# Optimization experiments

Measured on AMD Instinct MI355X. Metric: run time of the kernel, lower is better.

Reference implementation:

```python
import jax, jax.numpy as jnp
import numpy as np

EPS = 1e-6


def sparsemax(z):
    # sparsemax over last axis (Martins & Astudillo 2016)
    n = z.shape[-1]
    zs = -jnp.sort(-z, axis=-1)                      # sorted descending
    cum = jnp.cumsum(zs, axis=-1)
    k = jnp.arange(1, n + 1, dtype=z.dtype)
    support = (1.0 + k * zs) > cum                   # [..., n]
    ksup = jnp.sum(support, axis=-1, keepdims=True)  # support size (int)
    tau = (jnp.take_along_axis(cum, ksup - 1, axis=-1) - 1.0) / ksup.astype(z.dtype)
    return jnp.maximum(z - tau, 0.0)


def setup_inputs() -> dict:
    key = jax.random.key(0)
    k1, k2, k3, k4, k5, k6 = jax.random.split(key, 6)
    bi, bt, K, L, d = 128, 128, 36, 50, 1024
    img_cls = jax.random.normal(k1, (bi, d), dtype=jnp.float32)
    imgs = jax.random.normal(k2, (bi, K, d), dtype=jnp.float32)
    cap_cls = jax.random.normal(k3, (bt, d), dtype=jnp.float32)
    caps = jax.random.normal(k4, (bt, L, d), dtype=jnp.float32)
    img_lens = jax.random.randint(k5, (bi,), 18, K + 1).at[0].set(K)
    cap_lens = jax.random.randint(k6, (bt,), 25, L + 1).at[0].set(L)
    return {"img_cls": img_cls, "imgs": imgs, "cap_cls": cap_cls,
            "caps": caps, "img_lens": img_lens, "cap_lens": cap_lens}


def reference(img_cls, imgs, cap_cls, caps, img_lens, cap_lens):
    # forward_s2d: masked fine-grained sims -> sparsemax over flattened (K*L) -> weighted sum
    bi, K, d = imgs.shape
    bt, L, _ = caps.shape
    imgs = imgs + EPS
    caps = caps + EPS
    imgs = imgs / jnp.linalg.norm(imgs, axis=-1, keepdims=True)
    caps = caps / jnp.linalg.norm(caps, axis=-1, keepdims=True)
    fg = jnp.einsum('ikd,tld->itkl', imgs, caps)             # [bi,bt,K,L]
    rmask = jnp.arange(K)[None, :] < img_lens[:, None]        # [bi,K]
    cmask = jnp.arange(L)[None, :] < cap_lens[:, None]        # [bt,L]
    mask = rmask[:, None, :, None] & cmask[None, :, None, :]  # [bi,bt,K,L]
    fg = jnp.where(mask, fg, 0.0).reshape(bi, bt, K * L)
    attn = sparsemax(fg)
    return jnp.sum(fg * attn, axis=-1)                        # [bi,bt]
```

## Files before the change

kernel.cpp:

```cpp
#include <hip/hip_runtime.h>
#include <stdint.h>

#define EPSF 1e-6f

typedef unsigned short u16;
typedef __attribute__((ext_vector_type(8))) u16 u16x8;
typedef __attribute__((ext_vector_type(8))) __bf16 bf16x8;
typedef __attribute__((ext_vector_type(4))) float f32x4;

static constexpr int NBI = 128, NBT = 128, KI = 36, LC = 50, DD = 1024;
static constexpr int NEL = KI * LC;
static constexpr int GM  = NBI * KI;
static constexpr int GN  = NBT * LC;
static constexpr int BM = 256, BN = 256, BK = 64;
static constexpr int KT  = DD / BK;
static constexpr int MT  = GM / BM;
static constexpr int NTT = GN / BN;
static constexpr int TB  = BM * BK;

static __device__ __forceinline__ u16 f2bf(float f) {
  uint32_t u = __float_as_uint(f);
  u += 0x7fffu + ((u >> 16) & 1u);
  return (u16)(u >> 16);
}
static __device__ __forceinline__ float bf2f(u16 h) {
  return __uint_as_float((uint32_t)h << 16);
}

typedef __attribute__((address_space(1))) void gv_t;
typedef __attribute__((address_space(3))) void lv_t;
static __device__ __forceinline__ void gload16(const void* g, void* l) {
  __builtin_amdgcn_global_load_lds((const gv_t*)g, (lv_t*)l, 16, 0, 0);
}

__global__ __launch_bounds__(256) void hcam_normcast(
    const float* __restrict__ imgs, const float* __restrict__ caps,
    u16* __restrict__ A, u16* __restrict__ B) {
  int r = blockIdx.x;
  const float* src; u16* dst;
  if (r < GM) { src = imgs + (size_t)r * DD;        dst = A + (size_t)r * DD; }
  else        { src = caps + (size_t)(r - GM) * DD; dst = B + (size_t)(r - GM) * DD; }
  int tid = threadIdx.x;
  float4 v = *(const float4*)(src + tid * 4);
  v.x += EPSF; v.y += EPSF; v.z += EPSF; v.w += EPSF;
  float ss = v.x * v.x + v.y * v.y + v.z * v.z + v.w * v.w;
  #pragma unroll
  for (int m = 32; m; m >>= 1) ss += __shfl_xor(ss, m);
  __shared__ float wsum[4];
  if ((tid & 63) == 0) wsum[tid >> 6] = ss;
  __syncthreads();
  float inv = 1.0f / sqrtf(wsum[0] + wsum[1] + wsum[2] + wsum[3]);
  ushort4 o = make_ushort4(f2bf(v.x * inv), f2bf(v.y * inv), f2bf(v.z * inv), f2bf(v.w * inv));
  *(ushort4*)(dst + tid * 4) = o;
}

__global__ __launch_bounds__(512, 2) void hcam_gemm8(
    const u16* __restrict__ A, const u16* __restrict__ B, float* __restrict__ C) {
  __shared__ u16 As[2 * TB];
  __shared__ u16 Bs[2 * TB];

  const int nwg = MT * NTT;
  int orig = blockIdx.x;
  int qq = nwg >> 3, rr = nwg & 7;
  int xcd = orig & 7, idx = orig >> 3;
  int wg = (xcd < rr ? xcd * (qq + 1) : rr * (qq + 1) + (xcd - rr) * qq) + idx;
  const int bm = wg % MT, bn = wg / MT;

  const int tid = threadIdx.x, lane = tid & 63, w = tid >> 6;
  const int wm = w >> 2, wn = w & 3;
  const u16* Ag = A + (size_t)(bm * BM) * DD;
  const u16* Bg = B + (size_t)(bn * BN) * DD;

  const int srow = tid >> 3;
  const int sc16 = (tid & 7) ^ (srow & 7);
  const int wbase = w * 8;

  auto stage = [&](const u16* g, u16* lds, int kt, int h) {
    #pragma unroll
    for (int j = 0; j < 2; ++j) {
      int row = h * 128 + j * 64 + srow;
      gload16(g + (size_t)row * DD + kt * BK + sc16 * 8,
              lds + (h * 128 + j * 64 + wbase) * BK);
    }
  };

  f32x4 acc[8][4];
  #pragma unroll
  for (int i = 0; i < 8; ++i)
    #pragma unroll
    for (int j = 0; j < 4; ++j) acc[i][j] = (f32x4){0.f, 0.f, 0.f, 0.f};

  const int fr = lane & 15, g4 = lane >> 4;

  auto tile = [&](int t, u16* as_c, u16* bs_c, u16* as_n, u16* bs_n) {
    const int tn = t + 1;
    if (tn < KT) {
      stage(Ag, as_n, tn, 0);
      asm volatile("s_waitcnt vmcnt(2)" ::: "memory");
    } else {
      asm volatile("s_waitcnt vmcnt(0)" ::: "memory");
    }
    __builtin_amdgcn_s_barrier();
    __builtin_amdgcn_sched_barrier(0);
    #pragma unroll
    for (int ph = 0; ph < 4; ++ph) {
      const int mh = (ph == 0 || ph == 3) ? 0 : 1;
      const int nh = (ph >= 2) ? 1 : 0;
      bf16x8 af[2][4], bfv[2][2];
      #pragma unroll
      for (int k2 = 0; k2 < 2; ++k2) {
        const int c16 = k2 * 4 + g4;
        const int cs = (c16 ^ (fr & 7)) << 3;
        #pragma unroll
        for (int mi = 0; mi < 4; ++mi) {
          int rowl = wm * 128 + mh * 64 + mi * 16 + fr;
          af[k2][mi] = __builtin_bit_cast(bf16x8, *(const u16x8*)(as_c + rowl * BK + cs));
        }
        #pragma unroll
        for (int ni = 0; ni < 2; ++ni) {
          int rowl = wn * 64 + nh * 32 + ni * 16 + fr;
          bfv[k2][ni] = __builtin_bit_cast(bf16x8, *(const u16x8*)(bs_c + rowl * BK + cs));
        }
      }
      if (tn < KT) {
        if (ph == 0)      stage(Bg, bs_n, tn, 0);
        else if (ph == 1) stage(Ag, as_n, tn, 1);
        else if (ph == 2) stage(Bg, bs_n, tn, 1);
      }
      __builtin_amdgcn_s_setprio(1);
      #pragma unroll
      for (int k2 = 0; k2 < 2; ++k2)
        #pragma unroll
        for (int mi = 0; mi < 4; ++mi)
          #pragma unroll
          for (int ni = 0; ni < 2; ++ni)
            acc[mh * 4 + mi][nh * 2 + ni] = __builtin_amdgcn_mfma_f32_16x16x32_bf16(
                af[k2][mi], bfv[k2][ni], acc[mh * 4 + mi][nh * 2 + ni], 0, 0, 0);
      __builtin_amdgcn_s_setprio(0);
    }
    __builtin_amdgcn_s_barrier();
    __builtin_amdgcn_sched_barrier(0);
  };

  stage(Ag, As, 0, 0); stage(Ag, As, 0, 1);
  stage(Bg, Bs, 0, 0); stage(Bg, Bs, 0, 1);

  #pragma unroll 1
  for (int tp = 0; tp < KT; tp += 2) {
    tile(tp,     As,      Bs,      As + TB, Bs + TB);
    tile(tp + 1, As + TB, Bs + TB, As,      Bs);
  }

  const int fc = lane & 15, fq = (lane >> 4) * 4;
  #pragma unroll
  for (int am = 0; am < 8; ++am) {
    #pragma unroll
    for (int an = 0; an < 4; ++an) {
      const int row0 = bm * BM + wm * 128 + am * 16 + fq;
      const int col  = bn * BN + wn * 64 + an * 16 + fc;
      #pragma unroll
      for (int j = 0; j < 4; ++j)
        C[(size_t)(row0 + j) * GN + col] = acc[am][an][j];
    }
  }
}

static constexpr int RPT = (NEL + 63) / 64;

__global__ __launch_bounds__(256) void hcam_spmax_w(
    const float* __restrict__ C, const int* __restrict__ ilen, const int* __restrict__ clen,
    float* __restrict__ out) {
  const int wid  = blockIdx.x * 4 + (threadIdx.x >> 6);
  const int lane = threadIdx.x & 63;
  const int i = wid >> 7, t = wid & 127;
  const int il = ilen[i], cl = clen[t];
  const float* base = C + (size_t)i * KI * GN + t * LC;

  float v[RPT];
  float sum = 0.f;
  #pragma unroll
  for (int r = 0; r < RPT; ++r) {
    int p = lane + (r << 6);
    float x = -1e30f;
    if (p < NEL) {
      int k = p / LC, l = p - k * LC;
      if (k < il && l < cl) { x = base[(size_t)k * GN + l]; sum += x; }
    }
    v[r] = x;
  }
  #pragma unroll
  for (int m = 32; m; m >>= 1) sum += __shfl_xor(sum, m);

  const float mzero = (float)(NEL - il * cl);
  float tau  = (sum - 1.0f) * (1.0f / NEL);
  float prev = (float)NEL;
  for (int it = 0; it < 32; ++it) {
    float ss = 0.f, cc = 0.f;
    #pragma unroll
    for (int r = 0; r < RPT; ++r) {
      if (v[r] > tau) { ss += v[r]; cc += 1.0f; }
    }
    #pragma unroll
    for (int m = 32; m; m >>= 1) { ss += __shfl_xor(ss, m); cc += __shfl_xor(cc, m); }
    if (tau < 0.f) cc += mzero;
    if (cc == prev || cc < 1.0f) break;
    float tn = (ss - 1.0f) / cc;
    prev = cc;
    if (tn <= tau) break;
    tau = tn;
  }

  float o = 0.f;
  #pragma unroll
  for (int r = 0; r < RPT; ++r) {
    float d = v[r] - tau;
    if (d > 0.f) o += v[r] * d;
  }
  #pragma unroll
  for (int m = 32; m; m >>= 1) o += __shfl_xor(o, m);
  if (lane == 0) out[wid] = o;
}

static __device__ __forceinline__ void bred2(float& a, float& b2, int tid, float* red) {
  #pragma unroll
  for (int m = 32; m; m >>= 1) { a += __shfl_xor(a, m); b2 += __shfl_xor(b2, m); }
  __syncthreads();
  if ((tid & 63) == 0) { red[(tid >> 6) * 2] = a; red[(tid >> 6) * 2 + 1] = b2; }
  __syncthreads();
  a  = red[0] + red[2] + red[4] + red[6];
  b2 = red[1] + red[3] + red[5] + red[7];
}

static __device__ __forceinline__ void sparsemax_out(float vals[8], int tid, float* red, float* outp) {
  float s = 0.f, d = 0.f;
  #pragma unroll
  for (int r = 0; r < 8; ++r) { int p = tid + (r << 8); if (p < NEL) s += vals[r]; }
  bred2(s, d, tid, red);
  float tau  = (s - 1.0f) * (1.0f / NEL);
  float prev = (float)NEL;
  for (int it = 0; it < 64; ++it) {
    float ss = 0.f, cc = 0.f;
    #pragma unroll
    for (int r = 0; r < 8; ++r) {
      int p = tid + (r << 8);
      if (p < NEL && vals[r] > tau) { ss += vals[r]; cc += 1.0f; }
    }
    bred2(ss, cc, tid, red);
    if (cc == prev || cc < 1.0f) break;
    float tn = (ss - 1.0f) / cc;
    prev = cc;
    if (tn <= tau) break;
    tau = tn;
  }
  float o = 0.f; d = 0.f;
  #pragma unroll
  for (int r = 0; r < 8; ++r) {
    float v = vals[r], a2 = v - tau;
    if (a2 > 0.f) o += v * a2;
  }
  bred2(o, d, tid, red);
  if (tid == 0) *outp = o;
}

__global__ __launch_bounds__(256) void hcam_fused_bf(
    const u16* __restrict__ A, const u16* __restrict__ B,
    const int* __restrict__ ilen, const int* __restrict__ clen, float* __restrict__ out) {
  const int b = blockIdx.x;
  const int i = b >> 7, t = b & 127;
  const int tid = threadIdx.x;
  const int il = ilen[i], cl = clen[t];
  float vals[8];
  #pragma unroll
  for (int r = 0; r < 8; ++r) {
    int p = tid + (r << 8);
    float v = 0.f;
    if (p < NEL) {
      int k = p / LC, l = p - k * LC;
      if (k < il && l < cl) {
        const u16* ar = A + (size_t)(i * KI + k) * DD;
        const u16* br = B + (size_t)(t * LC + l) * DD;
        float s = 0.f;
        for (int dd = 0; dd < DD; dd += 8) {
          u16x8 av = *(const u16x8*)(ar + dd);
          u16x8 bv = *(const u16x8*)(br + dd);
          #pragma unroll
          for (int q = 0; q < 8; ++q) s += bf2f(av[q]) * bf2f(bv[q]);
        }
        v = s;
      }
    }
    vals[r] = v;
  }
  __shared__ float red[8];
  sparsemax_out(vals, tid, red, &out[b]);
}

__global__ __launch_bounds__(256) void hcam_fused_raw(
    const float* __restrict__ imgs, const float* __restrict__ caps,
    const int* __restrict__ ilen, const int* __restrict__ clen, float* __restrict__ out) {
  const int b = blockIdx.x;
  const int i = b >> 7, t = b & 127;
  const int tid = threadIdx.x;
  const int w = tid >> 6, lane = tid & 63;
  __shared__ float inv[KI + LC];
  for (int row = w; row < KI + LC; row += 4) {
    const float* src = (row < KI) ? imgs + (size_t)(i * KI + row) * DD
                                  : caps + (size_t)(t * LC + (row - KI)) * DD;
    float ss = 0.f;
    for (int e = lane; e < DD; e += 64) { float x = src[e] + EPSF; ss += x * x; }
    #pragma unroll
    for (int m = 32; m; m >>= 1) ss += __shfl_xor(ss, m);
    if (lane == 0) inv[row] = 1.0f / sqrtf(ss);
  }
  __syncthreads();
  const int il = ilen[i], cl = clen[t];
  float vals[8];
  #pragma unroll
  for (int r = 0; r < 8; ++r) {
    int p = tid + (r << 8);
    float v = 0.f;
    if (p < NEL) {
      int k = p / LC, l = p - k * LC;
      if (k < il && l < cl) {
        const float* ar = imgs + (size_t)(i * KI + k) * DD;
        const float* br = caps + (size_t)(t * LC + l) * DD;
        float s = 0.f;
        for (int dd = 0; dd < DD; dd += 4) {
          float4 a4 = *(const float4*)(ar + dd);
          float4 b4 = *(const float4*)(br + dd);
          s += (a4.x + EPSF) * (b4.x + EPSF) + (a4.y + EPSF) * (b4.y + EPSF)
             + (a4.z + EPSF) * (b4.z + EPSF) + (a4.w + EPSF) * (b4.w + EPSF);
        }
        v = s * inv[k] * inv[KI + l];
      }
    }
    vals[r] = v;
  }
  __shared__ float red[8];
  sparsemax_out(vals, tid, red, &out[b]);
}

extern "C" void kernel_launch(void* const* d_in, const int* in_sizes, int n_in,
                              void* d_out, int out_size, void* d_ws, size_t ws_size,
                              hipStream_t stream) {
  (void)in_sizes; (void)n_in; (void)out_size;
  const float* imgs = (const float*)d_in[1];
  const float* caps = (const float*)d_in[3];
  const int*   ilen = (const int*)d_in[4];
  const int*   clen = (const int*)d_in[5];
  float* out = (float*)d_out;

  const size_t offB     = (size_t)GM * DD * sizeof(u16);
  const size_t offC     = offB + (size_t)GN * DD * sizeof(u16);
  const size_t needFull = offC + (size_t)GM * GN * sizeof(float);
  u16*   A = (u16*)d_ws;
  u16*   B = (u16*)((char*)d_ws + offB);
  float* C = (float*)((char*)d_ws + offC);

  if (ws_size >= needFull) {
    hcam_normcast<<<dim3(GM + GN), dim3(256), 0, stream>>>(imgs, caps, A, B);
    hcam_gemm8<<<dim3(MT * NTT), dim3(512), 0, stream>>>(A, B, C);
    hcam_spmax_w<<<dim3(NBI * NBT / 4), dim3(256), 0, stream>>>(C, ilen, clen, out);
  } else if (ws_size >= offC) {
    hcam_normcast<<<dim3(GM + GN), dim3(256), 0, stream>>>(imgs, caps, A, B);
    hcam_fused_bf<<<dim3(NBI * NBT), dim3(256), 0, stream>>>(A, B, ilen, clen, out);
  } else {
    hcam_fused_raw<<<dim3(NBI * NBT), dim3(256), 0, stream>>>(imgs, caps, ilen, clen, out);
  }
}
```

Measured before the change: 132.2 us.

## Deepen GEMM prefetch pipeline with per-phase barriers and early A-tile staging

Restructures the double-buffered GEMM main loop so the first half of the A tile for step t+2 is prefetched during the last phase of step t, rather than at the start of the next tile. Barriers and LDS waits now sit inside each phase, so the MFMA work is no longer preceded by a blocking global-load wait at each tile boundary. The aim is to hide global-to-LDS latency more fully. In exchange it adds a block-wide barrier to every phase, and it writes into the buffer currently being read, which relies on those barriers for correctness.

```diff
diff --git a/kernel.cpp b/kernel.cpp
--- a/kernel.cpp
+++ b/kernel.cpp
@@ -92,16 +92,16 @@
 
   const int fr = lane & 15, g4 = lane >> 4;
 
-  auto tile = [&](int t, u16* as_c, u16* bs_c, u16* as_n, u16* bs_n) {
+  stage(Ag, As, 0, 0); stage(Bg, Bs, 0, 0);
+  stage(Ag, As, 0, 1); stage(Bg, Bs, 0, 1);
+  stage(Ag, As + TB, 1, 0);
+  asm volatile("s_waitcnt vmcnt(2)" ::: "memory");
+  __builtin_amdgcn_s_barrier();
+  __builtin_amdgcn_sched_barrier(0);
+
+  auto tile = [&](int t, u16* as_c, u16* bs_c, u16* as_n, u16* bs_n,
+                  u16* as_n2) {
     const int tn = t + 1;
-    if (tn < KT) {
-      stage(Ag, as_n, tn, 0);
-      asm volatile("s_waitcnt vmcnt(2)" ::: "memory");
-    } else {
-      asm volatile("s_waitcnt vmcnt(0)" ::: "memory");
-    }
-    __builtin_amdgcn_s_barrier();
-    __builtin_amdgcn_sched_barrier(0);
     #pragma unroll
     for (int ph = 0; ph < 4; ++ph) {
       const int mh = (ph == 0 || ph == 3) ? 0 : 1;
@@ -122,11 +122,14 @@
           bfv[k2][ni] = __builtin_bit_cast(bf16x8, *(const u16x8*)(bs_c + rowl * BK + cs));
         }
       }
-      if (tn < KT) {
-        if (ph == 0)      stage(Bg, bs_n, tn, 0);
-        else if (ph == 1) stage(Ag, as_n, tn, 1);
-        else if (ph == 2) stage(Bg, bs_n, tn, 1);
-      }
+      if (ph == 0 && tn < KT)      stage(Bg, bs_n, tn, 0);
+      else if (ph == 1 && tn < KT) stage(Ag, as_n, tn, 1);
+      else if (ph == 2 && tn < KT) stage(Bg, bs_n, tn, 1);
+      else if (ph == 3 && t + 2 < KT) stage(Ag, as_n2, t + 2, 0);
+
+      __builtin_amdgcn_s_barrier();
+      asm volatile("s_waitcnt lgkmcnt(0)" ::: "memory");
+      __builtin_amdgcn_sched_barrier(0);
       __builtin_amdgcn_s_setprio(1);
       #pragma unroll
       for (int k2 = 0; k2 < 2; ++k2)
@@ -137,18 +140,19 @@
             acc[mh * 4 + mi][nh * 2 + ni] = __builtin_amdgcn_mfma_f32_16x16x32_bf16(
                 af[k2][mi], bfv[k2][ni], acc[mh * 4 + mi][nh * 2 + ni], 0, 0, 0);
       __builtin_amdgcn_s_setprio(0);
-    }
-    __builtin_amdgcn_s_barrier();
-    __builtin_amdgcn_sched_barrier(0);
+      if (ph == 3) {
+        if (t + 2 < KT) { asm volatile("s_waitcnt vmcnt(2)" ::: "memory"); }
+        else            { asm volatile("s_waitcnt vmcnt(0)" ::: "memory"); }
+      }
+      __builtin_amdgcn_s_barrier();
+      __builtin_amdgcn_sched_barrier(0);
+    }
   };
-
-  stage(Ag, As, 0, 0); stage(Ag, As, 0, 1);
-  stage(Bg, Bs, 0, 0); stage(Bg, Bs, 0, 1);
 
   #pragma unroll 1
   for (int tp = 0; tp < KT; tp += 2) {
-    tile(tp,     As,      Bs,      As + TB, Bs + TB);
-    tile(tp + 1, As + TB, Bs + TB, As,      Bs);
+    tile(tp,     As,      Bs,      As + TB, Bs + TB, As);
+    tile(tp + 1, As + TB, Bs + TB, As,      Bs,      As + TB);
   }
 
   const int fc = lane & 15, fq = (lane >> 4) * 4;
```

New measurement: 146.7 us. +10.9%, slower.

## Store GEMM similarity matrix as fp16 and use 16-wave GEMM blocks

Applied to the files above, without the earlier changes.

The intermediate similarity matrix C is now written as fp16 instead of fp32, halving the memory traffic the GEMM epilogue writes and the sparsemax kernel reads. The GEMM moves from 512 to 1024 threads per block, so each wave owns a 64x64 sub-tile, each thread issues one staged global load per half-tile, and there is one resident block per CU. The first K tile is peeled out of the loop into a prologue. fp16 storage lowers the precision of the similarity values fed into sparsemax, and the larger block changes occupancy and register pressure.

```diff
diff --git a/kernel.cpp b/kernel.cpp
--- a/kernel.cpp
+++ b/kernel.cpp
@@ -54,8 +54,8 @@
   *(ushort4*)(dst + tid * 4) = o;
 }
 
-__global__ __launch_bounds__(512, 2) void hcam_gemm8(
-    const u16* __restrict__ A, const u16* __restrict__ B, float* __restrict__ C) {
+__global__ __launch_bounds__(1024, 1) void hcam_gemm16(
+    const u16* __restrict__ A, const u16* __restrict__ B, _Float16* __restrict__ C) {
   __shared__ u16 As[2 * TB];
   __shared__ u16 Bs[2 * TB];
 
@@ -76,17 +76,13 @@
   const int wbase = w * 8;
 
   auto stage = [&](const u16* g, u16* lds, int kt, int h) {
-    #pragma unroll
-    for (int j = 0; j < 2; ++j) {
-      int row = h * 128 + j * 64 + srow;
-      gload16(g + (size_t)row * DD + kt * BK + sc16 * 8,
-              lds + (h * 128 + j * 64 + wbase) * BK);
-    }
+    gload16(g + (size_t)(h * 128 + srow) * DD + kt * BK + sc16 * 8,
+            lds + (h * 128 + wbase) * BK);
   };
 
-  f32x4 acc[8][4];
-  #pragma unroll
-  for (int i = 0; i < 8; ++i)
+  f32x4 acc[4][4];
+  #pragma unroll
+  for (int i = 0; i < 4; ++i)
     #pragma unroll
     for (int j = 0; j < 4; ++j) acc[i][j] = (f32x4){0.f, 0.f, 0.f, 0.f};
 
@@ -96,7 +92,7 @@
     const int tn = t + 1;
     if (tn < KT) {
       stage(Ag, as_n, tn, 0);
-      asm volatile("s_waitcnt vmcnt(2)" ::: "memory");
+      asm volatile("s_waitcnt vmcnt(1)" ::: "memory");
     } else {
       asm volatile("s_waitcnt vmcnt(0)" ::: "memory");
     }
@@ -106,14 +102,14 @@
     for (int ph = 0; ph < 4; ++ph) {
       const int mh = (ph == 0 || ph == 3) ? 0 : 1;
       const int nh = (ph >= 2) ? 1 : 0;
-      bf16x8 af[2][4], bfv[2][2];
+      bf16x8 af[2][2], bfv[2][2];
       #pragma unroll
       for (int k2 = 0; k2 < 2; ++k2) {
         const int c16 = k2 * 4 + g4;
         const int cs = (c16 ^ (fr & 7)) << 3;
         #pragma unroll
-        for (int mi = 0; mi < 4; ++mi) {
-          int rowl = wm * 128 + mh * 64 + mi * 16 + fr;
+        for (int mi = 0; mi < 2; ++mi) {
+          int rowl = wm * 64 + mh * 32 + mi * 16 + fr;
           af[k2][mi] = __builtin_bit_cast(bf16x8, *(const u16x8*)(as_c + rowl * BK + cs));
         }
         #pragma unroll
@@ -131,36 +127,79 @@
       #pragma unroll
       for (int k2 = 0; k2 < 2; ++k2)
         #pragma unroll
-        for (int mi = 0; mi < 4; ++mi)
+        for (int mi = 0; mi < 2; ++mi)
           #pragma unroll
           for (int ni = 0; ni < 2; ++ni)
-            acc[mh * 4 + mi][nh * 2 + ni] = __builtin_amdgcn_mfma_f32_16x16x32_bf16(
-                af[k2][mi], bfv[k2][ni], acc[mh * 4 + mi][nh * 2 + ni], 0, 0, 0);
+            acc[mh * 2 + mi][nh * 2 + ni] = __builtin_amdgcn_mfma_f32_16x16x32_bf16(
+                af[k2][mi], bfv[k2][ni], acc[mh * 2 + mi][nh * 2 + ni], 0, 0, 0);
       __builtin_amdgcn_s_setprio(0);
     }
     __builtin_amdgcn_s_barrier();
     __builtin_amdgcn_sched_barrier(0);
   };
 
-  stage(Ag, As, 0, 0); stage(Ag, As, 0, 1);
-  stage(Bg, Bs, 0, 0); stage(Bg, Bs, 0, 1);
+  stage(Ag, As, 0, 0); stage(Bg, Bs, 0, 0);
+  stage(Ag, As, 0, 1); stage(Bg, Bs, 0, 1);
+  stage(Ag, As + TB, 1, 0);
+  {
+    asm volatile("s_waitcnt vmcnt(1)" ::: "memory");
+    __builtin_amdgcn_s_barrier();
+    __builtin_amdgcn_sched_barrier(0);
+    #pragma unroll
+    for (int ph = 0; ph < 4; ++ph) {
+      const int mh = (ph == 0 || ph == 3) ? 0 : 1;
+      const int nh = (ph >= 2) ? 1 : 0;
+      bf16x8 af[2][2], bfv[2][2];
+      #pragma unroll
+      for (int k2 = 0; k2 < 2; ++k2) {
+        const int c16 = k2 * 4 + g4;
+        const int cs = (c16 ^ (fr & 7)) << 3;
+        #pragma unroll
+        for (int mi = 0; mi < 2; ++mi) {
+          int rowl = wm * 64 + mh * 32 + mi * 16 + fr;
+          af[k2][mi] = __builtin_bit_cast(bf16x8, *(const u16x8*)(As + rowl * BK + cs));
+        }
+        #pragma unroll
+        for (int ni = 0; ni < 2; ++ni) {
+          int rowl = wn * 64 + nh * 32 + ni * 16 + fr;
+          bfv[k2][ni] = __builtin_bit_cast(bf16x8, *(const u16x8*)(Bs + rowl * BK + cs));
+        }
+      }
+      if (ph == 0)      stage(Bg, Bs + TB, 1, 0);
+      else if (ph == 1) stage(Ag, As + TB, 1, 1);
+      else if (ph == 2) stage(Bg, Bs + TB, 1, 1);
+      __builtin_amdgcn_s_setprio(1);
+      #pragma unroll
+      for (int k2 = 0; k2 < 2; ++k2)
+        #pragma unroll
+        for (int mi = 0; mi < 2; ++mi)
+          #pragma unroll
+          for (int ni = 0; ni < 2; ++ni)
+            acc[mh * 2 + mi][nh * 2 + ni] = __builtin_amdgcn_mfma_f32_16x16x32_bf16(
+                af[k2][mi], bfv[k2][ni], acc[mh * 2 + mi][nh * 2 + ni], 0, 0, 0);
+      __builtin_amdgcn_s_setprio(0);
+    }
+    __builtin_amdgcn_s_barrier();
+    __builtin_amdgcn_sched_barrier(0);
+  }
 
   #pragma unroll 1
-  for (int tp = 0; tp < KT; tp += 2) {
-    tile(tp,     As,      Bs,      As + TB, Bs + TB);
-    tile(tp + 1, As + TB, Bs + TB, As,      Bs);
-  }
+  for (int tp = 1; tp + 1 < KT; tp += 2) {
+    tile(tp,     As + TB, Bs + TB, As,      Bs);
+    tile(tp + 1, As,      Bs,      As + TB, Bs + TB);
+  }
+  tile(KT - 1, As + TB, Bs + TB, As, Bs);
 
   const int fc = lane & 15, fq = (lane >> 4) * 4;
   #pragma unroll
-  for (int am = 0; am < 8; ++am) {
+  for (int am = 0; am < 4; ++am) {
     #pragma unroll
     for (int an = 0; an < 4; ++an) {
-      const int row0 = bm * BM + wm * 128 + am * 16 + fq;
+      const int row0 = bm * BM + wm * 64 + am * 16 + fq;
       const int col  = bn * BN + wn * 64 + an * 16 + fc;
       #pragma unroll
       for (int j = 0; j < 4; ++j)
-        C[(size_t)(row0 + j) * GN + col] = acc[am][an][j];
+        C[(size_t)(row0 + j) * GN + col] = (_Float16)acc[am][an][j];
     }
   }
 }
@@ -168,13 +207,13 @@
 static constexpr int RPT = (NEL + 63) / 64;
 
 __global__ __launch_bounds__(256) void hcam_spmax_w(
-    const float* __restrict__ C, const int* __restrict__ ilen, const int* __restrict__ clen,
+    const _Float16* __restrict__ C, const int* __restrict__ ilen, const int* __restrict__ clen,
     float* __restrict__ out) {
   const int wid  = blockIdx.x * 4 + (threadIdx.x >> 6);
   const int lane = threadIdx.x & 63;
   const int i = wid >> 7, t = wid & 127;
   const int il = ilen[i], cl = clen[t];
-  const float* base = C + (size_t)i * KI * GN + t * LC;
+  const _Float16* base = C + (size_t)i * KI * GN + t * LC;
 
   float v[RPT];
   float sum = 0.f;
@@ -184,7 +223,7 @@
     float x = -1e30f;
     if (p < NEL) {
       int k = p / LC, l = p - k * LC;
-      if (k < il && l < cl) { x = base[(size_t)k * GN + l]; sum += x; }
+      if (k < il && l < cl) { x = (float)base[(size_t)k * GN + l]; sum += x; }
     }
     v[r] = x;
   }
@@ -352,14 +391,14 @@
 
   const size_t offB     = (size_t)GM * DD * sizeof(u16);
   const size_t offC     = offB + (size_t)GN * DD * sizeof(u16);
-  const size_t needFull = offC + (size_t)GM * GN * sizeof(float);
-  u16*   A = (u16*)d_ws;
-  u16*   B = (u16*)((char*)d_ws + offB);
-  float* C = (float*)((char*)d_ws + offC);
+  const size_t needFull = offC + (size_t)GM * GN * sizeof(_Float16);
+  u16*      A = (u16*)d_ws;
+  u16*      B = (u16*)((char*)d_ws + offB);
+  _Float16* C = (_Float16*)((char*)d_ws + offC);
 
   if (ws_size >= needFull) {
     hcam_normcast<<<dim3(GM + GN), dim3(256), 0, stream>>>(imgs, caps, A, B);
-    hcam_gemm8<<<dim3(MT * NTT), dim3(512), 0, stream>>>(A, B, C);
+    hcam_gemm16<<<dim3(MT * NTT), dim3(1024), 0, stream>>>(A, B, C);
     hcam_spmax_w<<<dim3(NBI * NBT / 4), dim3(256), 0, stream>>>(C, ilen, clen, out);
   } else if (ws_size >= offC) {
     hcam_normcast<<<dim3(GM + GN), dim3(256), 0, stream>>>(imgs, caps, A, B);
```

Measured after the change: 127.4 us. 1.04x faster.
